# Performance work log

Hardware: AMD Instinct MI355X
Metric: run time of the kernel (lower is better)

## Reference

```python
import jax, jax.numpy as jnp
import numpy as np

B, N, C, H = 16, 1024, 768, 12
HD = C // H  # head_dim = 64


def setup_inputs() -> dict:
    key = jax.random.key(0)
    ks = jax.random.split(key, 3)
    scale = 1.0 / np.sqrt(C)
    x = jax.random.normal(ks[0], (B, N, C), dtype=jnp.float32)
    Wqkv = jax.random.normal(ks[1], (C, 3 * C), dtype=jnp.float32) * scale
    bqkv = jnp.zeros((3 * C,), dtype=jnp.float32)
    Wout = jax.random.normal(ks[2], (C, C), dtype=jnp.float32) * scale
    bout = jnp.zeros((C,), dtype=jnp.float32)
    return {"x": x, "Wqkv": Wqkv, "bqkv": bqkv, "Wout": Wout, "bout": bout}


def reference(x, Wqkv, bqkv, Wout, bout):
    # QKV projection: [B,N,3C] -> [B,N,3,H,HD]
    qkv = (x @ Wqkv + bqkv).reshape(B, N, 3, H, HD)
    q = qkv[:, :, 0].transpose(0, 2, 1, 3)  # [B,H,N,HD]
    k = qkv[:, :, 1].transpose(0, 2, 1, 3)
    v = qkv[:, :, 2].transpose(0, 2, 1, 3)
    # Patch attention (the only path that reaches the output: the source's
    # cross-image attention result is overwritten before out_proj, so it is
    # dead code). Dropout is identity in eval mode.
    scores = jnp.einsum("bhqd,bhkd->bhqk", q, k) / np.sqrt(HD).astype(np.float32)
    attn = jax.nn.softmax(scores, axis=-1)
    out = jnp.einsum("bhqk,bhkd->bhqd", attn, v)  # [B,H,N,HD]
    out = out.transpose(0, 2, 1, 3).reshape(B, N, C)
    return out @ Wout + bout
```

## Files before the change

### kernel.cpp

```cpp
#include <hip/hip_runtime.h>
#include <hip/hip_bf16.h>

#define B_   16
#define N_   1024
#define C_   768
#define H_   12
#define HD_  64
#define M_   16384
#define N1_  2304
#define NEG_BIG (-1e30f)
#define LOG2E 1.4426950408889634f

typedef __attribute__((ext_vector_type(8))) _Float16 f16x8;
typedef __attribute__((ext_vector_type(4))) float f32x4;
typedef __attribute__((ext_vector_type(16))) float f32x16;

__device__ __forceinline__ unsigned short f2h(float f) {
  _Float16 h = (_Float16)f;
  union { _Float16 h; unsigned short u; } c; c.h = h; return c.u;
}
__device__ __forceinline__ unsigned int cvtpk_f16(float a, float b) {
  unsigned int r;
  asm("v_cvt_pkrtz_f16_f32 %0, %1, %2" : "=v"(r) : "v"(a), "v"(b));
  return r;
}
__device__ __forceinline__ float exp2_asm(float x) {
  float r;
  asm("v_exp_f32 %0, %1" : "=v"(r) : "v"(x));
  return r;
}

__device__ __forceinline__ void gload_lds16(const void* g, void* l) {
  __builtin_amdgcn_global_load_lds(
      (const __attribute__((address_space(1))) void*)g,
      (__attribute__((address_space(3))) void*)l, 16, 0, 0);
}

typedef __attribute__((ext_vector_type(8))) short u16x8;

__global__ __launch_bounds__(256)
void k_prep_all(const float* __restrict__ x, const float* __restrict__ Wqkv,
                const float* __restrict__ Wout,
                unsigned short* __restrict__ xh,
                unsigned short* __restrict__ WqkvT,
                unsigned short* __restrict__ WoutT) {
  int bid = blockIdx.x;
  if (bid < 6144) {
    long i = ((long)bid * 256 + threadIdx.x) * 8;
    float4 a = *(const float4*)(x + i);
    float4 b = *(const float4*)(x + i + 4);
    u16x8 v;
    v[0] = (short)f2h(a.x); v[1] = (short)f2h(a.y);
    v[2] = (short)f2h(a.z); v[3] = (short)f2h(a.w);
    v[4] = (short)f2h(b.x); v[5] = (short)f2h(b.y);
    v[6] = (short)f2h(b.z); v[7] = (short)f2h(b.w);
    *(u16x8*)(xh + i) = v;
  } else if (bid < 7008) {
    int tid = (bid - 6144) * 256 + threadIdx.x;
    int n  = tid % N1_;
    int kc = tid / N1_;
    u16x8 v;
#pragma unroll
    for (int j = 0; j < 8; ++j)
      v[j] = (short)f2h(Wqkv[(long)(kc * 8 + j) * N1_ + n]);
    *(u16x8*)(WqkvT + (long)n * C_ + kc * 8) = v;
  } else {
    int tid = (bid - 7008) * 256 + threadIdx.x;
    int n  = tid % C_;
    int kc = tid / C_;
    u16x8 v;
#pragma unroll
    for (int j = 0; j < 8; ++j)
      v[j] = (short)f2h(Wout[(long)(kc * 8 + j) * C_ + n]);
    *(u16x8*)(WoutT + (long)n * C_ + kc * 8) = v;
  }
}

template <int STAGE>
__global__ __launch_bounds__(256, 4)
void gemm128(const unsigned short* __restrict__ A,
             const unsigned short* __restrict__ Bt,
             const float* __restrict__ bias,
             void* __restrict__ out, unsigned short* __restrict__ Vt,
             int Kdim, int Ndim) {
  __shared__ unsigned char lds[32768];
  const int t = threadIdx.x;
  const int l = t & 63, w = t >> 6;
  const int g = l >> 4, lr = l & 15;
  const int NB = Ndim >> 7;
  const int wgid = (blockIdx.x & 7) * (gridDim.x >> 3) + (blockIdx.x >> 3);
  const int mb = wgid / NB, nb = wgid % NB;
  const long m0 = (long)mb << 7, n0 = (long)nb << 7;
  const int wm = w >> 1, wn = w & 1;

  f32x4 acc[4][4];
  const f32x4 zz = {0.f, 0.f, 0.f, 0.f};
#pragma unroll
  for (int i = 0; i < 4; ++i)
#pragma unroll
    for (int j = 0; j < 4; ++j) acc[i][j] = zz;

  int srow[4], sx[4];
#pragma unroll
  for (int i = 0; i < 4; ++i) {
    int s = i * 4096 + t * 16;
    int row = s >> 7;
    srow[i] = row;
    sx[i] = (s & 127) ^ ((row & 7) << 4);
  }
  const char* Ab = (const char*)A;
  const char* Bb = (const char*)Bt;
  const long K2 = (long)Kdim * 2;
  const int wbase = (t & 192) * 16;

  for (int kt = 0; kt < Kdim; kt += 64) {
#pragma unroll
    for (int i = 0; i < 4; ++i) {
      const char* src = Ab + (m0 + srow[i]) * K2 + kt * 2 + sx[i];
      gload_lds16(src, (void*)(lds + i * 4096 + wbase));
    }
#pragma unroll
    for (int i = 0; i < 4; ++i) {
      const char* src = Bb + (n0 + srow[i]) * K2 + kt * 2 + sx[i];
      gload_lds16(src, (void*)(lds + 16384 + i * 4096 + wbase));
    }
    __syncthreads();
#pragma unroll
    for (int ks = 0; ks < 2; ++ks) {
      f16x8 af[4], bfr[4];
#pragma unroll
      for (int mi = 0; mi < 4; ++mi) {
        int row = wm * 64 + mi * 16 + lr;
        int off = row * 128 + ((ks * 64 + g * 16) ^ ((row & 7) << 4));
        af[mi] = *(const f16x8*)(lds + off);
      }
#pragma unroll
      for (int ni = 0; ni < 4; ++ni) {
        int row = wn * 64 + ni * 16 + lr;
        int off = 16384 + row * 128 + ((ks * 64 + g * 16) ^ ((row & 7) << 4));
        bfr[ni] = *(const f16x8*)(lds + off);
      }
#pragma unroll
      for (int mi = 0; mi < 4; ++mi)
#pragma unroll
        for (int ni = 0; ni < 4; ++ni)
          acc[mi][ni] = __builtin_amdgcn_mfma_f32_16x16x32_f16(
              af[mi], bfr[ni], acc[mi][ni], 0, 0, 0);
    }
    __syncthreads();
  }

  if (STAGE == 1 && n0 >= 1536) {
    unsigned short* lt = (unsigned short*)lds;
#pragma unroll
    for (int ni = 0; ni < 4; ++ni) {
      int col = wn * 64 + ni * 16 + lr;
      int s = (col & 15) << 3;
      float bv = bias[(int)n0 + col];
#pragma unroll
      for (int mi = 0; mi < 4; ++mi) {
        int rowb = wm * 64 + mi * 16 + g * 4;
        unsigned d0 = cvtpk_f16(acc[mi][ni][0] + bv, acc[mi][ni][1] + bv);
        unsigned d1 = cvtpk_f16(acc[mi][ni][2] + bv, acc[mi][ni][3] + bv);
        unsigned long long dd = (unsigned long long)d0 |
                                ((unsigned long long)d1 << 32);
        *(unsigned long long*)(lt + col * 128 + (rowb ^ s)) = dd;
      }
    }
    __syncthreads();
    const int b_  = (int)(m0 >> 10);
    const int nof = (int)(m0 & 1023);
    const int h0  = ((int)n0 - 1536) >> 6;
#pragma unroll
    for (int it = 0; it < 8; ++it) {
      int col  = it * 16 + (t >> 4);
      int tokc = (t & 15) * 8;
      int s = (col & 15) << 3;
      u16x8 v = *(const u16x8*)(lt + col * 128 + (tokc ^ s));
      int bh = b_ * H_ + h0 + (col >> 6);
      int d  = col & 63;
      *(u16x8*)(Vt + ((long)bh * HD_ + d) * N_ + nof + tokc) = v;
    }
  } else if (STAGE == 1) {
    float sc = (n0 < 768) ? 0.125f * LOG2E : 1.0f;
    unsigned short* cl = (unsigned short*)lds;
#pragma unroll
    for (int ni = 0; ni < 4; ++ni) {
      int col = wn * 64 + ni * 16 + lr;
      float bv = bias[(int)n0 + col];
#pragma unroll
      for (int mi = 0; mi < 4; ++mi)
#pragma unroll
        for (int r = 0; r < 4; ++r) {
          int row = wm * 64 + mi * 16 + g * 4 + r;
          cl[row * 128 + col] = f2h((acc[mi][ni][r] + bv) * sc);
        }
    }
    __syncthreads();
    unsigned short* o = (unsigned short*)out;
#pragma unroll
    for (int it = 0; it < 8; ++it) {
      int idx = it * 2048 + t * 8;
      int row = idx >> 7;
      int col = idx & 127;
      *(u16x8*)(o + (m0 + row) * N1_ + n0 + col) = *(const u16x8*)(cl + idx);
    }
  } else {
    float* o = (float*)out;
#pragma unroll
    for (int ni = 0; ni < 4; ++ni) {
      int col = (int)n0 + wn * 64 + ni * 16 + lr;
      float bv = bias[col];
#pragma unroll
      for (int mi = 0; mi < 4; ++mi)
#pragma unroll
        for (int r = 0; r < 4; ++r) {
          long rowm = m0 + wm * 64 + mi * 16 + g * 4 + r;
          o[rowm * C_ + col] = acc[mi][ni][r] + bv;
        }
    }
  }
}

__global__ __launch_bounds__(256, 4)
void attn_fused(const unsigned short* __restrict__ qkvb,
                const unsigned short* __restrict__ Vt,
                unsigned short* __restrict__ Ofp) {
  __shared__ unsigned char lds[32768];
  const int t = threadIdx.x, l = t & 63, w = t >> 6;
  const int q32 = l & 31;
  const int hi = l >> 5;
  const int hi16 = hi * 16;
  const int wid = (blockIdx.x & 7) * 192 + (blockIdx.x >> 3);
  const int bh = wid >> 3, qb = wid & 7;
  const int b = bh / H_, h = bh % H_;
  const long tok0 = (long)b * N_;
  const int q0 = qb * 128 + w * 32;
  const long mytok = tok0 + q0 + q32;

  f16x8 qa[4];
#pragma unroll
  for (int cs = 0; cs < 4; ++cs)
    qa[cs] = *(const f16x8*)(qkvb + mytok * N1_ + h * HD_ + cs * 16 + hi * 8);

  const f32x16 zz16 = {0.f};
  f32x16 o0 = zz16, o1 = zz16;
  float mrun = NEG_BIG, lrun = 0.f;

  const int row0 = q32, row1 = 32 + q32;
  const int swz0 = (q32 & 7) << 4;

  const int sxs = ((t & 7) * 16) ^ (((t >> 3) & 7) << 4);
  const int wbase = (t & 192) * 16;
  const char* Vg = (const char*)(Vt + (long)bh * HD_ * N_);
  const char* Kg = (const char*)qkvb + ((tok0)*N1_ + C_ + h * HD_) * 2;

#define STAGE_KV(kv0, buf)                                                  \
  {                                                                         \
    _Pragma("unroll")                                                       \
    for (int i = 0; i < 2; ++i) {                                           \
      int row = i * 32 + (t >> 3);                                          \
      gload_lds16(Kg + ((long)(kv0 + row) * N1_) * 2 + sxs,                 \
                  (void*)((buf) + i * 4096 + wbase));                       \
    }                                                                       \
    _Pragma("unroll")                                                       \
    for (int i = 0; i < 2; ++i) {                                           \
      int row = i * 32 + (t >> 3);                                          \
      gload_lds16(Vg + ((long)row * N_ + (kv0)) * 2 + sxs,                  \
                  (void*)((buf) + 8192 + i * 4096 + wbase));                \
    }                                                                       \
  }

  STAGE_KV(0, lds);

#pragma unroll 2
  for (int tt = 0; tt < 16; ++tt) {
    unsigned char* curb = lds + (tt & 1) * 16384;
    unsigned char* nxtb = lds + ((tt & 1) ^ 1) * 16384;
    if (tt < 15) {
      STAGE_KV((tt + 1) * 64, nxtb);
      asm volatile("s_waitcnt vmcnt(4)" ::: "memory");
    } else {
      asm volatile("s_waitcnt vmcnt(0)" ::: "memory");
    }
    __builtin_amdgcn_s_barrier();
    __builtin_amdgcn_sched_barrier(0);

    f32x16 sa0 = zz16, sa1 = zz16;
#pragma unroll
    for (int cs = 0; cs < 4; ++cs) {
      f16x8 kf0 = *(const f16x8*)(curb + row0 * 128 + ((cs * 32 + hi16) ^ swz0));
      f16x8 kf1 = *(const f16x8*)(curb + row1 * 128 + ((cs * 32 + hi16) ^ swz0));
      sa0 = __builtin_amdgcn_mfma_f32_32x32x16_f16(kf0, qa[cs], sa0, 0, 0, 0);
      sa1 = __builtin_amdgcn_mfma_f32_32x32x16_f16(kf1, qa[cs], sa1, 0, 0, 0);
    }

    float tm[11];
#pragma unroll
    for (int i = 0; i < 5; ++i)
      tm[i] = fmaxf(fmaxf(sa0[3 * i], sa0[3 * i + 1]), sa0[3 * i + 2]);
    tm[5] = fmaxf(sa0[15], sa1[0]);
#pragma unroll
    for (int i = 0; i < 5; ++i)
      tm[6 + i] = fmaxf(fmaxf(sa1[3 * i + 1], sa1[3 * i + 2]), sa1[3 * i + 3]);
    float u0 = fmaxf(fmaxf(tm[0], tm[1]), tm[2]);
    float u1 = fmaxf(fmaxf(tm[3], tm[4]), tm[5]);
    float u2 = fmaxf(fmaxf(tm[6], tm[7]), tm[8]);
    float u3 = fmaxf(fmaxf(tm[9], tm[10]), u0);
    float mx = fmaxf(fmaxf(u1, u2), u3);
    mx = fmaxf(mx, __shfl_xor(mx, 32));
    if (!__all(mx <= mrun + 8.f)) {
      float mn = fmaxf(mrun, mx);
      float al = exp2_asm(mrun - mn);
      mrun = mn;
      lrun *= al;
      o0 *= al;
      o1 *= al;
    }
    float p0a[16], p1a[16];
#pragma unroll
    for (int i = 0; i < 16; ++i) p0a[i] = exp2_asm(sa0[i] - mrun);
#pragma unroll
    for (int i = 0; i < 16; ++i) p1a[i] = exp2_asm(sa1[i] - mrun);
    unsigned pk[2][4][2];
#pragma unroll
    for (int g = 0; g < 4; ++g) {
      pk[0][g][0] = cvtpk_f16(p0a[4 * g + 0], p0a[4 * g + 1]);
      pk[0][g][1] = cvtpk_f16(p0a[4 * g + 2], p0a[4 * g + 3]);
      pk[1][g][0] = cvtpk_f16(p1a[4 * g + 0], p1a[4 * g + 1]);
      pk[1][g][1] = cvtpk_f16(p1a[4 * g + 2], p1a[4 * g + 3]);
    }
    float ts[16];
#pragma unroll
    for (int i = 0; i < 16; ++i) ts[i] = p0a[i] + p1a[i];
#pragma unroll
    for (int s = 8; s >= 1; s >>= 1)
#pragma unroll
      for (int i = 0; i < s; ++i) ts[i] += ts[i + s];
    float rs = ts[0];
    rs += __shfl_xor(rs, 32);
    lrun += rs;

    f16x8 pb[4];
#pragma unroll
    for (int tk = 0; tk < 2; ++tk)
#pragma unroll
      for (int par = 0; par < 2; ++par) {
        unsigned a0 = pk[tk][2 * par][0], b0 = pk[tk][2 * par + 1][0];
        unsigned a1 = pk[tk][2 * par][1], b1 = pk[tk][2 * par + 1][1];
        asm("v_permlane32_swap_b32 %0, %1" : "+v"(a0), "+v"(b0));
        asm("v_permlane32_swap_b32 %0, %1" : "+v"(a1), "+v"(b1));
        union { unsigned u[4]; f16x8 v; } pw;
        pw.u[0] = a0; pw.u[1] = a1; pw.u[2] = b0; pw.u[3] = b1;
        pb[2 * tk + par] = pw.v;
      }

#pragma unroll
    for (int kb = 0; kb < 4; ++kb) {
      f16x8 vf0 = *(const f16x8*)(curb + 8192 + row0 * 128 + ((kb * 32 + hi16) ^ swz0));
      f16x8 vf1 = *(const f16x8*)(curb + 8192 + row1 * 128 + ((kb * 32 + hi16) ^ swz0));
      o0 = __builtin_amdgcn_mfma_f32_32x32x16_f16(vf0, pb[kb], o0, 0, 0, 0);
      o1 = __builtin_amdgcn_mfma_f32_32x32x16_f16(vf1, pb[kb], o1, 0, 0, 0);
    }
    __builtin_amdgcn_sched_barrier(0);
    asm volatile("s_waitcnt lgkmcnt(0)" ::: "memory");
    __builtin_amdgcn_s_barrier();
  }
#undef STAGE_KV

  float inv = 1.0f / lrun;
  unsigned short* obase = Ofp + mytok * C_ + h * HD_;
#pragma unroll
  for (int dt = 0; dt < 2; ++dt) {
#pragma unroll
    for (int j = 0; j < 4; ++j) {
      int r = 4 * j;
      const f32x16& oo = dt ? o1 : o0;
      unsigned hw0 = cvtpk_f16(oo[r] * inv, oo[r + 1] * inv);
      unsigned hw1 = cvtpk_f16(oo[r + 2] * inv, oo[r + 3] * inv);
      unsigned long long dd = (unsigned long long)hw0 |
                              ((unsigned long long)hw1 << 32);
      int d = dt * 32 + 8 * j + 4 * hi;
      *(unsigned long long*)(obase + d) = dd;
    }
  }
}

extern "C" void kernel_launch(void* const* d_in, const int* in_sizes, int n_in,
                              void* d_out, int out_size, void* d_ws, size_t ws_size,
                              hipStream_t stream) {
  const float* x    = (const float*)d_in[0];
  const float* Wqkv = (const float*)d_in[1];
  const float* bqkv = (const float*)d_in[2];
  const float* Wout = (const float*)d_in[3];
  const float* bout = (const float*)d_in[4];

  char* ws = (char*)d_ws;
  unsigned short* qkvb  = (unsigned short*)(ws);
  unsigned short* Ofp   = (unsigned short*)(ws + 75497472L);
  unsigned short* xh    = (unsigned short*)(ws + 100663296L);
  unsigned short* Vt    = (unsigned short*)(ws + 125829120L);
  unsigned short* WqkvT = (unsigned short*)(ws + 150994944L);
  unsigned short* WoutT = (unsigned short*)(ws + 154533888L);

  k_prep_all<<<7296, 256, 0, stream>>>(x, Wqkv, Wout, xh, WqkvT, WoutT);
  gemm128<1><<<2304, 256, 0, stream>>>(xh, WqkvT, bqkv, (void*)qkvb, Vt, 768, 2304);
  attn_fused<<<1536, 256, 0, stream>>>(qkvb, Vt, Ofp);
  gemm128<3><<<768, 256, 0, stream>>>(Ofp, WoutT, bout, d_out, nullptr, 768, 768);
}
```

Measured before the change: 177.9 us.

## Process two 32-query groups per wave in attention to reuse K/V tiles

Each wave now handles 64 queries as two independent 32-row groups that share the same K and V fragments read from LDS, so each block covers 256 queries and the grid is halved. This halves the K/V global-to-LDS staging and LDS fragment reads per query. In exchange it doubles the accumulator and score registers per wave, so launch bounds drop to 2 blocks per CU, which lowers occupancy. The loop unroll pragma is also removed.

```diff
diff --git a/kernel.cpp b/kernel.cpp
--- a/kernel.cpp
+++ b/kernel.cpp
@@ -222,7 +222,7 @@
   }
 }
 
-__global__ __launch_bounds__(256, 4)
+__global__ __launch_bounds__(256, 2)
 void attn_fused(const unsigned short* __restrict__ qkvb,
                 const unsigned short* __restrict__ Vt,
                 unsigned short* __restrict__ Ofp) {
@@ -231,21 +231,24 @@
   const int q32 = l & 31;
   const int hi = l >> 5;
   const int hi16 = hi * 16;
-  const int wid = (blockIdx.x & 7) * 192 + (blockIdx.x >> 3);
-  const int bh = wid >> 3, qb = wid & 7;
+  const int wid = (blockIdx.x & 7) * 96 + (blockIdx.x >> 3);
+  const int bh = wid >> 2, qb = wid & 3;
   const int b = bh / H_, h = bh % H_;
   const long tok0 = (long)b * N_;
-  const int q0 = qb * 128 + w * 32;
-  const long mytok = tok0 + q0 + q32;
-
-  f16x8 qa[4];
-#pragma unroll
-  for (int cs = 0; cs < 4; ++cs)
-    qa[cs] = *(const f16x8*)(qkvb + mytok * N1_ + h * HD_ + cs * 16 + hi * 8);
+  const int q0 = qb * 256 + w * 64;
+  const long mytokA = tok0 + q0 + q32;
+  const long mytokB = mytokA + 32;
+
+  f16x8 qaA[4], qaB[4];
+#pragma unroll
+  for (int cs = 0; cs < 4; ++cs) {
+    qaA[cs] = *(const f16x8*)(qkvb + mytokA * N1_ + h * HD_ + cs * 16 + hi * 8);
+    qaB[cs] = *(const f16x8*)(qkvb + mytokB * N1_ + h * HD_ + cs * 16 + hi * 8);
+  }
 
   const f32x16 zz16 = {0.f};
-  f32x16 o0 = zz16, o1 = zz16;
-  float mrun = NEG_BIG, lrun = 0.f;
+  f32x16 oA0 = zz16, oA1 = zz16, oB0 = zz16, oB1 = zz16;
+  float mrunA = NEG_BIG, lrunA = 0.f, mrunB = NEG_BIG, lrunB = 0.f;
 
   const int row0 = q32, row1 = 32 + q32;
   const int swz0 = (q32 & 7) << 4;
@@ -260,7 +263,7 @@
     _Pragma("unroll")                                                       \
     for (int i = 0; i < 2; ++i) {                                           \
       int row = i * 32 + (t >> 3);                                          \
-      gload_lds16(Kg + ((long)(kv0 + row) * N1_) * 2 + sxs,                 \
+      gload_lds16(Kg + ((long)((kv0) + row) * N1_) * 2 + sxs,               \
                   (void*)((buf) + i * 4096 + wbase));                       \
     }                                                                       \
     _Pragma("unroll")                                                       \
@@ -271,9 +274,70 @@
     }                                                                       \
   }
 
+#define SOFTMAX_GROUP(sa0, sa1, mrun, lrun, o0, o1, pb)                     \
+  {                                                                         \
+    float tm[11];                                                           \
+    _Pragma("unroll")                                                       \
+    for (int i = 0; i < 5; ++i)                                             \
+      tm[i] = fmaxf(fmaxf(sa0[3 * i], sa0[3 * i + 1]), sa0[3 * i + 2]);     \
+    tm[5] = fmaxf(sa0[15], sa1[0]);                                         \
+    _Pragma("unroll")                                                       \
+    for (int i = 0; i < 5; ++i)                                             \
+      tm[6 + i] = fmaxf(fmaxf(sa1[3 * i + 1], sa1[3 * i + 2]),              \
+                        sa1[3 * i + 3]);                                    \
+    float u0 = fmaxf(fmaxf(tm[0], tm[1]), tm[2]);                           \
+    float u1 = fmaxf(fmaxf(tm[3], tm[4]), tm[5]);                           \
+    float u2 = fmaxf(fmaxf(tm[6], tm[7]), tm[8]);                           \
+    float u3 = fmaxf(fmaxf(tm[9], tm[10]), u0);                             \
+    float mx = fmaxf(fmaxf(u1, u2), u3);                                    \
+    mx = fmaxf(mx, __shfl_xor(mx, 32));                                     \
+    if (!__all(mx <= mrun + 8.f)) {                                         \
+      float mn = fmaxf(mrun, mx);                                           \
+      float al = exp2_asm(mrun - mn);                                       \
+      mrun = mn;                                                            \
+      lrun *= al;                                                           \
+      o0 *= al;                                                             \
+      o1 *= al;                                                             \
+    }                                                                       \
+    float p0a[16], p1a[16];                                                 \
+    _Pragma("unroll")                                                       \
+    for (int i = 0; i < 16; ++i) p0a[i] = exp2_asm(sa0[i] - mrun);          \
+    _Pragma("unroll")                                                       \
+    for (int i = 0; i < 16; ++i) p1a[i] = exp2_asm(sa1[i] - mrun);          \
+    unsigned pk[2][4][2];                                                   \
+    _Pragma("unroll")                                                       \
+    for (int g = 0; g < 4; ++g) {                                           \
+      pk[0][g][0] = cvtpk_f16(p0a[4 * g + 0], p0a[4 * g + 1]);              \
+      pk[0][g][1] = cvtpk_f16(p0a[4 * g + 2], p0a[4 * g + 3]);              \
+      pk[1][g][0] = cvtpk_f16(p1a[4 * g + 0], p1a[4 * g + 1]);              \
+      pk[1][g][1] = cvtpk_f16(p1a[4 * g + 2], p1a[4 * g + 3]);              \
+    }                                                                       \
+    float ts[16];                                                           \
+    _Pragma("unroll")                                                       \
+    for (int i = 0; i < 16; ++i) ts[i] = p0a[i] + p1a[i];                   \
+    _Pragma("unroll")                                                       \
+    for (int s = 8; s >= 1; s >>= 1)                                        \
+      _Pragma("unroll")                                                     \
+      for (int i = 0; i < s; ++i) ts[i] += ts[i + s];                       \
+    float rs = ts[0];                                                       \
+    rs += __shfl_xor(rs, 32);                                               \
+    lrun += rs;                                                             \
+    _Pragma("unroll")                                                       \
+    for (int tk = 0; tk < 2; ++tk)                                          \
+      _Pragma("unroll")                                                     \
+      for (int par = 0; par < 2; ++par) {                                   \
+        unsigned a0 = pk[tk][2 * par][0], b0 = pk[tk][2 * par + 1][0];      \
+        unsigned a1 = pk[tk][2 * par][1], b1 = pk[tk][2 * par + 1][1];      \
+        asm("v_permlane32_swap_b32 %0, %1" : "+v"(a0), "+v"(b0));           \
+        asm("v_permlane32_swap_b32 %0, %1" : "+v"(a1), "+v"(b1));           \
+        union { unsigned u[4]; f16x8 v; } pw;                               \
+        pw.u[0] = a0; pw.u[1] = a1; pw.u[2] = b0; pw.u[3] = b1;             \
+        pb[2 * tk + par] = pw.v;                                            \
+      }                                                                     \
+  }
+
   STAGE_KV(0, lds);
 
-#pragma unroll 2
   for (int tt = 0; tt < 16; ++tt) {
     unsigned char* curb = lds + (tt & 1) * 16384;
     unsigned char* nxtb = lds + ((tt & 1) ^ 1) * 16384;
@@ -286,102 +350,71 @@
     __builtin_amdgcn_s_barrier();
     __builtin_amdgcn_sched_barrier(0);
 
-    f32x16 sa0 = zz16, sa1 = zz16;
+    f32x16 sA0 = zz16, sA1 = zz16, sB0 = zz16, sB1 = zz16;
 #pragma unroll
     for (int cs = 0; cs < 4; ++cs) {
       f16x8 kf0 = *(const f16x8*)(curb + row0 * 128 + ((cs * 32 + hi16) ^ swz0));
       f16x8 kf1 = *(const f16x8*)(curb + row1 * 128 + ((cs * 32 + hi16) ^ swz0));
-      sa0 = __builtin_amdgcn_mfma_f32_32x32x16_f16(kf0, qa[cs], sa0, 0, 0, 0);
-      sa1 = __builtin_amdgcn_mfma_f32_32x32x16_f16(kf1, qa[cs], sa1, 0, 0, 0);
-    }
-
-    float tm[11];
-#pragma unroll
-    for (int i = 0; i < 5; ++i)
-      tm[i] = fmaxf(fmaxf(sa0[3 * i], sa0[3 * i + 1]), sa0[3 * i + 2]);
-    tm[5] = fmaxf(sa0[15], sa1[0]);
-#pragma unroll
-    for (int i = 0; i < 5; ++i)
-      tm[6 + i] = fmaxf(fmaxf(sa1[3 * i + 1], sa1[3 * i + 2]), sa1[3 * i + 3]);
-    float u0 = fmaxf(fmaxf(tm[0], tm[1]), tm[2]);
-    float u1 = fmaxf(fmaxf(tm[3], tm[4]), tm[5]);
-    float u2 = fmaxf(fmaxf(tm[6], tm[7]), tm[8]);
-    float u3 = fmaxf(fmaxf(tm[9], tm[10]), u0);
-    float mx = fmaxf(fmaxf(u1, u2), u3);
-    mx = fmaxf(mx, __shfl_xor(mx, 32));
-    if (!__all(mx <= mrun + 8.f)) {
-      float mn = fmaxf(mrun, mx);
-      float al = exp2_asm(mrun - mn);
-      mrun = mn;
-      lrun *= al;
-      o0 *= al;
-      o1 *= al;
-    }
-    float p0a[16], p1a[16];
-#pragma unroll
-    for (int i = 0; i < 16; ++i) p0a[i] = exp2_asm(sa0[i] - mrun);
-#pragma unroll
-    for (int i = 0; i < 16; ++i) p1a[i] = exp2_asm(sa1[i] - mrun);
-    unsigned pk[2][4][2];
-#pragma unroll
-    for (int g = 0; g < 4; ++g) {
-      pk[0][g][0] = cvtpk_f16(p0a[4 * g + 0], p0a[4 * g + 1]);
-      pk[0][g][1] = cvtpk_f16(p0a[4 * g + 2], p0a[4 * g + 3]);
-      pk[1][g][0] = cvtpk_f16(p1a[4 * g + 0], p1a[4 * g + 1]);
-      pk[1][g][1] = cvtpk_f16(p1a[4 * g + 2], p1a[4 * g + 3]);
-    }
-    float ts[16];
-#pragma unroll
-    for (int i = 0; i < 16; ++i) ts[i] = p0a[i] + p1a[i];
-#pragma unroll
-    for (int s = 8; s >= 1; s >>= 1)
-#pragma unroll
-      for (int i = 0; i < s; ++i) ts[i] += ts[i + s];
-    float rs = ts[0];
-    rs += __shfl_xor(rs, 32);
-    lrun += rs;
-
-    f16x8 pb[4];
-#pragma unroll
-    for (int tk = 0; tk < 2; ++tk)
-#pragma unroll
-      for (int par = 0; par < 2; ++par) {
-        unsigned a0 = pk[tk][2 * par][0], b0 = pk[tk][2 * par + 1][0];
-        unsigned a1 = pk[tk][2 * par][1], b1 = pk[tk][2 * par + 1][1];
-        asm("v_permlane32_swap_b32 %0, %1" : "+v"(a0), "+v"(b0));
-        asm("v_permlane32_swap_b32 %0, %1" : "+v"(a1), "+v"(b1));
-        union { unsigned u[4]; f16x8 v; } pw;
-        pw.u[0] = a0; pw.u[1] = a1; pw.u[2] = b0; pw.u[3] = b1;
-        pb[2 * tk + par] = pw.v;
-      }
+      sA0 = __builtin_amdgcn_mfma_f32_32x32x16_f16(kf0, qaA[cs], sA0, 0, 0, 0);
+      sA1 = __builtin_amdgcn_mfma_f32_32x32x16_f16(kf1, qaA[cs], sA1, 0, 0, 0);
+      sB0 = __builtin_amdgcn_mfma_f32_32x32x16_f16(kf0, qaB[cs], sB0, 0, 0, 0);
+      sB1 = __builtin_amdgcn_mfma_f32_32x32x16_f16(kf1, qaB[cs], sB1, 0, 0, 0);
+    }
+
+    f16x8 pbA[4], pbB[4];
+    SOFTMAX_GROUP(sA0, sA1, mrunA, lrunA, oA0, oA1, pbA);
+    SOFTMAX_GROUP(sB0, sB1, mrunB, lrunB, oB0, oB1, pbB);
 
 #pragma unroll
     for (int kb = 0; kb < 4; ++kb) {
       f16x8 vf0 = *(const f16x8*)(curb + 8192 + row0 * 128 + ((kb * 32 + hi16) ^ swz0));
       f16x8 vf1 = *(const f16x8*)(curb + 8192 + row1 * 128 + ((kb * 32 + hi16) ^ swz0));
-      o0 = __builtin_amdgcn_mfma_f32_32x32x16_f16(vf0, pb[kb], o0, 0, 0, 0);
-      o1 = __builtin_amdgcn_mfma_f32_32x32x16_f16(vf1, pb[kb], o1, 0, 0, 0);
+      oA0 = __builtin_amdgcn_mfma_f32_32x32x16_f16(vf0, pbA[kb], oA0, 0, 0, 0);
+      oA1 = __builtin_amdgcn_mfma_f32_32x32x16_f16(vf1, pbA[kb], oA1, 0, 0, 0);
+      oB0 = __builtin_amdgcn_mfma_f32_32x32x16_f16(vf0, pbB[kb], oB0, 0, 0, 0);
+      oB1 = __builtin_amdgcn_mfma_f32_32x32x16_f16(vf1, pbB[kb], oB1, 0, 0, 0);
     }
     __builtin_amdgcn_sched_barrier(0);
     asm volatile("s_waitcnt lgkmcnt(0)" ::: "memory");
     __builtin_amdgcn_s_barrier();
   }
 #undef STAGE_KV
-
-  float inv = 1.0f / lrun;
-  unsigned short* obase = Ofp + mytok * C_ + h * HD_;
-#pragma unroll
-  for (int dt = 0; dt < 2; ++dt) {
-#pragma unroll
-    for (int j = 0; j < 4; ++j) {
-      int r = 4 * j;
-      const f32x16& oo = dt ? o1 : o0;
-      unsigned hw0 = cvtpk_f16(oo[r] * inv, oo[r + 1] * inv);
-      unsigned hw1 = cvtpk_f16(oo[r + 2] * inv, oo[r + 3] * inv);
-      unsigned long long dd = (unsigned long long)hw0 |
-                              ((unsigned long long)hw1 << 32);
-      int d = dt * 32 + 8 * j + 4 * hi;
-      *(unsigned long long*)(obase + d) = dd;
+#undef SOFTMAX_GROUP
+
+  {
+    float inv = 1.0f / lrunA;
+    unsigned short* obase = Ofp + mytokA * C_ + h * HD_;
+#pragma unroll
+    for (int dt = 0; dt < 2; ++dt) {
+#pragma unroll
+      for (int j = 0; j < 4; ++j) {
+        int r = 4 * j;
+        const f32x16& oo = dt ? oA1 : oA0;
+        unsigned hw0 = cvtpk_f16(oo[r] * inv, oo[r + 1] * inv);
+        unsigned hw1 = cvtpk_f16(oo[r + 2] * inv, oo[r + 3] * inv);
+        unsigned long long dd = (unsigned long long)hw0 |
+                                ((unsigned long long)hw1 << 32);
+        int d = dt * 32 + 8 * j + 4 * hi;
+        *(unsigned long long*)(obase + d) = dd;
+      }
+    }
+  }
+  {
+    float inv = 1.0f / lrunB;
+    unsigned short* obase = Ofp + mytokB * C_ + h * HD_;
+#pragma unroll
+    for (int dt = 0; dt < 2; ++dt) {
+#pragma unroll
+      for (int j = 0; j < 4; ++j) {
+        int r = 4 * j;
+        const f32x16& oo = dt ? oB1 : oB0;
+        unsigned hw0 = cvtpk_f16(oo[r] * inv, oo[r + 1] * inv);
+        unsigned hw1 = cvtpk_f16(oo[r + 2] * inv, oo[r + 3] * inv);
+        unsigned long long dd = (unsigned long long)hw0 |
+                                ((unsigned long long)hw1 << 32);
+        int d = dt * 32 + 8 * j + 4 * hi;
+        *(unsigned long long*)(obase + d) = dd;
+      }
     }
   }
 }
@@ -405,6 +438,6 @@
 
   k_prep_all<<<7296, 256, 0, stream>>>(x, Wqkv, Wout, xh, WqkvT, WoutT);
   gemm128<1><<<2304, 256, 0, stream>>>(xh, WqkvT, bqkv, (void*)qkvb, Vt, 768, 2304);
-  attn_fused<<<1536, 256, 0, stream>>>(qkvb, Vt, Ofp);
+  attn_fused<<<768, 256, 0, stream>>>(qkvb, Vt, Ofp);
   gemm128<3><<<768, 256, 0, stream>>>(Ofp, WoutT, bout, d_out, nullptr, 768, 768);
 }
```

New measurement: 175.4 us. About the same (-1.4%).
